# Kernel optimization log

Hardware: AMD Instinct MI355X
Metric: run time of the kernel (lower is better)

Reference implementation:

```python
import jax, jax.numpy as jnp
import numpy as np

N_NODES = 100000


def setup_inputs() -> dict:
    key = jax.random.key(0)
    k1, k2, k3, k4 = jax.random.split(key, 4)
    E = 1600000
    in_dim, out_dim = 256, 64
    h = jax.random.normal(k1, (N_NODES, in_dim), dtype=jnp.float32)
    src = jax.random.randint(k2, (E,), 0, N_NODES, dtype=jnp.int64)
    dst = jax.random.randint(k3, (E,), 0, N_NODES, dtype=jnp.int64)
    W = jax.random.normal(k4, (in_dim, out_dim), dtype=jnp.float32) * (1.0 / np.sqrt(in_dim))
    b = jnp.zeros((out_dim,), dtype=jnp.float32)
    return {"h": h, "src": src, "dst": dst, "W": W, "b": b}


def reference(h, src, dst, W, b):
    # dgl GraphConv, norm='both': out = D_in^{-1/2} A D_out^{-1/2} h W + b
    E = src.shape[0]
    ones = jnp.ones((E,), dtype=h.dtype)
    deg_out = jax.ops.segment_sum(ones, src, num_segments=N_NODES)  # out-degree of src nodes
    deg_in = jax.ops.segment_sum(ones, dst, num_segments=N_NODES)   # in-degree of dst nodes
    norm_src = jnp.clip(deg_out, 1.0, None) ** -0.5                  # [N]
    norm_dst = jnp.clip(deg_in, 1.0, None) ** -0.5                   # [N]
    # in_dim > out_dim: project first (as dgl does), then aggregate small features
    x = (h * norm_src[:, None]) @ W                                  # [N, out_dim]
    msgs = x[src]                                                    # [E, out_dim] gather
    agg = jax.ops.segment_sum(msgs, dst, num_segments=N_NODES)      # [N, out_dim] scatter-add
    out = agg * norm_dst[:, None] + b
    # ReLU; dropout is identity in eval mode
    return jax.nn.relu(out)
```

## Files before the change

### kernel.cpp

```cpp
#include <hip/hip_runtime.h>
#include <hip/hip_fp16.h>

#define N_NODES 100000
#define IN_DIM 256
#define OUT_DIM 64
#define NT 782
#define NSC 512
#define SMAX 3200
#define CAP_F 3072
#define GEMM_BLKS 1563

typedef _Float16 half8 __attribute__((ext_vector_type(8)));
typedef float f32x4 __attribute__((ext_vector_type(4)));

__global__ __launch_bounds__(256) void init_kernel(int* __restrict__ cursorD,
                                                   int* __restrict__ cursorS) {
    int i = blockIdx.x * 256 + threadIdx.x;
    if (i < NT) { cursorD[i] = 0; cursorS[i] = 0; }
}

#define A_LD 136
__global__ __launch_bounds__(256) void fused_kernel(const int* __restrict__ src,
                                                    const int* __restrict__ dst,
                                                    int* __restrict__ cursorD,
                                                    int* __restrict__ cursorS,
                                                    int* __restrict__ binnedD,
                                                    unsigned char* __restrict__ srcb,
                                                    const float* __restrict__ hmat,
                                                    const float* __restrict__ W,
                                                    __half* __restrict__ xh,
                                                    int E, int chunk) {
    __shared__ char smem[47568];
    const int t = threadIdx.x;
    if (blockIdx.x < NSC) {
        int* sorted            = (int*)(smem);
        int* histD             = (int*)(smem + 12800);
        int* boffD             = (int*)(smem + 15928);
        int* resvD             = (int*)(smem + 19056);
        int* histS             = (int*)(smem + 22184);
        int* boffS             = (int*)(smem + 25312);
        int* resvS             = (int*)(smem + 28440);
        unsigned short* sbin   = (unsigned short*)(smem + 31568);
        unsigned short* sbinS  = (unsigned short*)(smem + 37968);
        unsigned char* sortedB = (unsigned char*)(smem + 44368);
        const int blk = blockIdx.x;
        const int lane = t & 63, wv = t >> 6;
        const int lo = blk * chunk;
        int hiA = lo + chunk; if (hiA > E) hiA = E;
        for (int s0 = lo; s0 < hiA; s0 += SMAX) {
            int m = hiA - s0; if (m > SMAX) m = SMAX;
            for (int i = t; i < NT; i += 256) { histD[i] = 0; histS[i] = 0; }
            __syncthreads();
            for (int k = t; k < m; k += 256) {
                int s = src[s0 + k], d = dst[s0 + k];
                atomicAdd(&histD[d >> 7], 1);
                atomicAdd(&histS[s >> 7], 1);
            }
            __syncthreads();
            if (wv < 2) {
                int* hsrc = (wv == 0) ? histD : histS;
                int* bdst = (wv == 0) ? boffD : boffS;
                int carry = 0;
                for (int r = 0; r < (NT + 63) / 64; ++r) {
                    int i = r * 64 + lane;
                    int v = (i < NT) ? hsrc[i] : 0;
                    int incl = v;
#pragma unroll
                    for (int off = 1; off < 64; off <<= 1) {
                        int y = __shfl_up(incl, off);
                        if (lane >= off) incl += y;
                    }
                    if (i < NT) bdst[i] = carry + incl - v;
                    carry += __shfl(incl, 63);
                }
            }
            __syncthreads();
            for (int i = t; i < NT; i += 256) {
                int hd = histD[i];
                if (hd) resvD[i] = atomicAdd(&cursorD[i], hd);
                int hs = histS[i];
                if (hs) resvS[i] = atomicAdd(&cursorS[i], hs);
                histD[i] = boffD[i];
                histS[i] = boffS[i];
            }
            __syncthreads();
            for (int k = t; k < m; k += 256) {
                int s = src[s0 + k], d = dst[s0 + k];
                int bd = d >> 7;
                int p = atomicAdd(&histD[bd], 1);
                sorted[p] = (s << 7) | (d & 127);
                sbin[p] = (unsigned short)bd;
                int bs = s >> 7;
                int ps = atomicAdd(&histS[bs], 1);
                sortedB[ps] = (unsigned char)(s & 127);
                sbinS[ps] = (unsigned short)bs;
            }
            __syncthreads();
            for (int k = t; k < m; k += 256) {
                int b = sbin[k];
                int loc = resvD[b] + (k - boffD[b]);
                if (loc < CAP_F) binnedD[b * CAP_F + loc] = sorted[k];
                int bs = sbinS[k];
                int locS = resvS[bs] + (k - boffS[bs]);
                if (locS < CAP_F) srcb[bs * CAP_F + locS] = sortedB[k];
            }
            __syncthreads();
        }
    } else {
        _Float16* sA = (_Float16*)(smem);
        _Float16* sB = (_Float16*)(smem + 64 * A_LD * 2);
        const int lane = t & 63;
        const int w = t >> 6;
        const int row0 = (blockIdx.x - NSC) * 64;
        const int m0 = (w & 1) * 32;
        const int n0 = (w >> 1) * 32;

        f32x4 acc00 = {0.f, 0.f, 0.f, 0.f}, acc01 = {0.f, 0.f, 0.f, 0.f};
        f32x4 acc10 = {0.f, 0.f, 0.f, 0.f}, acc11 = {0.f, 0.f, 0.f, 0.f};

        for (int khalf = 0; khalf < 2; ++khalf) {
            const int k0 = khalf * 128;
            __syncthreads();
#pragma unroll
            for (int it = 0; it < 8; ++it) {
                int f = t + it * 256;
                int row = f >> 5;
                int c4 = f & 31;
                int grow = row0 + row; if (grow >= N_NODES) grow = N_NODES - 1;
                float4 v = *(const float4*)(hmat + (size_t)grow * IN_DIM + k0 + c4 * 4);
                _Float16 p[4];
                p[0] = (_Float16)v.x; p[1] = (_Float16)v.y;
                p[2] = (_Float16)v.z; p[3] = (_Float16)v.w;
                *(uint2*)&sA[row * A_LD + c4 * 4] = *(uint2*)p;
            }
            {
                int n = t & 63;
                int kk0 = (t >> 6) * 32;
#pragma unroll
                for (int kb = 0; kb < 8; ++kb) {
                    _Float16 p[4];
#pragma unroll
                    for (int u = 0; u < 4; ++u)
                        p[u] = (_Float16)W[(size_t)(k0 + kk0 + kb * 4 + u) * OUT_DIM + n];
                    *(uint2*)&sB[n * A_LD + kk0 + kb * 4] = *(uint2*)p;
                }
            }
            __syncthreads();
#pragma unroll
            for (int kb = 0; kb < 4; ++kb) {
                int koff = kb * 32 + (lane >> 4) * 8;
                half8 a0 = *(const half8*)&sA[(m0 + (lane & 15)) * A_LD + koff];
                half8 a1 = *(const half8*)&sA[(m0 + 16 + (lane & 15)) * A_LD + koff];
                half8 b0 = *(const half8*)&sB[(n0 + (lane & 15)) * A_LD + koff];
                half8 b1 = *(const half8*)&sB[(n0 + 16 + (lane & 15)) * A_LD + koff];
                acc00 = __builtin_amdgcn_mfma_f32_16x16x32_f16(a0, b0, acc00, 0, 0, 0);
                acc01 = __builtin_amdgcn_mfma_f32_16x16x32_f16(a0, b1, acc01, 0, 0, 0);
                acc10 = __builtin_amdgcn_mfma_f32_16x16x32_f16(a1, b0, acc10, 0, 0, 0);
                acc11 = __builtin_amdgcn_mfma_f32_16x16x32_f16(a1, b1, acc11, 0, 0, 0);
            }
        }

        const int col16 = lane & 15;
        const int rq = (lane >> 4) * 4;
#pragma unroll
        for (int mi = 0; mi < 2; ++mi) {
#pragma unroll
            for (int ni = 0; ni < 2; ++ni) {
                const f32x4 a = (mi == 0) ? (ni == 0 ? acc00 : acc01)
                                          : (ni == 0 ? acc10 : acc11);
                int col = n0 + ni * 16 + col16;
#pragma unroll
                for (int r = 0; r < 4; ++r) {
                    int row = row0 + m0 + mi * 16 + rq + r;
                    if (row < N_NODES)
                        xh[(size_t)row * OUT_DIM + col] = __float2half(a[r]);
                }
            }
        }
    }
}

__global__ __launch_bounds__(256) void tile_kernel(const int* __restrict__ cursorD,
                                                   const int* __restrict__ cursorS,
                                                   const int* __restrict__ binnedD,
                                                   const unsigned char* __restrict__ srcb,
                                                   int* __restrict__ csr,
                                                   int* __restrict__ offs, int* __restrict__ cnt,
                                                   float* __restrict__ nrmS) {
    __shared__ int h[128], cur[128];
    __shared__ int lcsr[CAP_F];
    __shared__ int w0tot;
    const int bin = blockIdx.x, t = threadIdx.x, lane = t & 63;
    if (t < 128) h[t] = 0;
    __syncthreads();

    const int base = bin * CAP_F;
    int m = cursorD[bin]; if (m > CAP_F) m = CAP_F;
    for (int k = t; k < m; k += 256) atomicAdd(&h[binnedD[base + k] & 127], 1);
    __syncthreads();
    int v = (t < 128) ? h[t] : 0;
    int incl = v;
#pragma unroll
    for (int off = 1; off < 64; off <<= 1) {
        int y = __shfl_up(incl, off);
        if (lane >= off) incl += y;
    }
    if (t == 63) w0tot = incl;
    __syncthreads();
    int excl = incl - v + ((t >= 64 && t < 128) ? w0tot : 0);
    if (t < 128) {
        cur[t] = excl;
        int node = bin * 128 + t;
        if (node < N_NODES) { offs[node] = base + excl; cnt[node] = v; }
    }
    __syncthreads();
    for (int k = t; k < m; k += 256) {
        int rec = binnedD[base + k];
        int p = atomicAdd(&cur[rec & 127], 1);
        lcsr[p] = rec >> 7;
    }
    __syncthreads();
    for (int k = t; k < m; k += 256) csr[base + k] = lcsr[k];

    __syncthreads();
    if (t < 128) h[t] = 0;
    __syncthreads();
    int ms = cursorS[bin]; if (ms > CAP_F) ms = CAP_F;
    const int sbase = bin * CAP_F;
    for (int k = t; k < ms; k += 256) atomicAdd(&h[srcb[sbase + k]], 1);
    __syncthreads();
    if (t < 128) {
        int node = bin * 128 + t;
        if (node < N_NODES) {
            int d = h[t];
            nrmS[node] = rsqrtf((float)(d < 1 ? 1 : d));
        }
    }
}

__global__ __launch_bounds__(256) void aggregate_kernel(const int* __restrict__ offs,
                                                        const int* __restrict__ cnt,
                                                        const int* __restrict__ csr,
                                                        const float* __restrict__ nrmS,
                                                        const __half* __restrict__ xh,
                                                        const float* __restrict__ b,
                                                        float* __restrict__ out) {
    const int t = threadIdx.x;
    const int lane = t & 63;
    const int wid = t >> 6;
    const int node = blockIdx.x * 4 + wid;
    const int g = lane >> 3;
    const int c = lane & 7;

    const int start = offs[node];
    const int n = cnt[node];

    float acc[8] = {0.f, 0.f, 0.f, 0.f, 0.f, 0.f, 0.f, 0.f};
    for (int base = 0; base < n; base += 64) {
        int k = base + lane;
        int sidx = (k < n) ? csr[start + k] : 0;
        int m = n - base; if (m > 64) m = 64;
        for (int e0 = 0; e0 < m; e0 += 16) {
            int ea = e0 + g;
            int eb = e0 + 8 + g;
            int sa = __shfl(sidx, ea);
            int sb = __shfl(sidx, eb);
            bool va = ea < m;
            bool vb = eb < m;
            float wa = va ? nrmS[sa] : 0.f;
            uint4 ra = *(const uint4*)(xh + (size_t)(va ? sa : 0) * OUT_DIM + 8 * c);
            const bool grpb = (e0 + 8) < m;
            uint4 rb;
            float wb = 0.f;
            if (grpb) {
                wb = vb ? nrmS[sb] : 0.f;
                rb = *(const uint4*)(xh + (size_t)(vb ? sb : 0) * OUT_DIM + 8 * c);
            }
            {
                const __half2* hp = (const __half2*)&ra;
#pragma unroll
                for (int p = 0; p < 4; ++p) {
                    float2 f = __half22float2(hp[p]);
                    acc[2 * p]     = fmaf(wa, f.x, acc[2 * p]);
                    acc[2 * p + 1] = fmaf(wa, f.y, acc[2 * p + 1]);
                }
            }
            if (grpb) {
                const __half2* hp = (const __half2*)&rb;
#pragma unroll
                for (int p = 0; p < 4; ++p) {
                    float2 f = __half22float2(hp[p]);
                    acc[2 * p]     = fmaf(wb, f.x, acc[2 * p]);
                    acc[2 * p + 1] = fmaf(wb, f.y, acc[2 * p + 1]);
                }
            }
        }
    }

#pragma unroll
    for (int off = 8; off < 64; off <<= 1) {
#pragma unroll
        for (int p = 0; p < 8; ++p)
            acc[p] += __shfl_xor(acc[p], off);
    }

    if (g == 0) {
        float nrm = rsqrtf((float)(n < 1 ? 1 : n));
        float4 bv0 = *(const float4*)&b[c * 8];
        float4 bv1 = *(const float4*)&b[c * 8 + 4];
        float4 r0, r1;
        r0.x = fmaxf(fmaf(acc[0], nrm, bv0.x), 0.f);
        r0.y = fmaxf(fmaf(acc[1], nrm, bv0.y), 0.f);
        r0.z = fmaxf(fmaf(acc[2], nrm, bv0.z), 0.f);
        r0.w = fmaxf(fmaf(acc[3], nrm, bv0.w), 0.f);
        r1.x = fmaxf(fmaf(acc[4], nrm, bv1.x), 0.f);
        r1.y = fmaxf(fmaf(acc[5], nrm, bv1.y), 0.f);
        r1.z = fmaxf(fmaf(acc[6], nrm, bv1.z), 0.f);
        r1.w = fmaxf(fmaf(acc[7], nrm, bv1.w), 0.f);
        float4* orow = (float4*)(out + (size_t)node * OUT_DIM + c * 8);
        orow[0] = r0;
        orow[1] = r1;
    }
}

extern "C" void kernel_launch(void* const* d_in, const int* in_sizes, int n_in,
                              void* d_out, int out_size, void* d_ws, size_t ws_size,
                              hipStream_t stream) {
    const float* h   = (const float*)d_in[0];
    const int*   src = (const int*)d_in[1];
    const int*   dst = (const int*)d_in[2];
    const float* W   = (const float*)d_in[3];
    const float* b   = (const float*)d_in[4];
    float* out = (float*)d_out;
    const int E = in_sizes[1];
    const int chunkS = (E + NSC - 1) / NSC;

    char* ws = (char*)d_ws;
    int*           cursorD = (int*)(ws);
    int*           cursorS = (int*)(ws + 3328);
    int*           binnedD = (int*)(ws + 6656);
    int*           csr     = binnedD;
    unsigned char* srcb    = (unsigned char*)(ws + 9615872);
    int*           offs    = (int*)(ws + 12018176);
    int*           cntA    = (int*)(ws + 12418176);
    float*         nrmS    = (float*)(ws + 12818176);
    __half*        xh      = (__half*)(ws + 13218176);

    init_kernel<<<4, 256, 0, stream>>>(cursorD, cursorS);
    fused_kernel<<<NSC + GEMM_BLKS, 256, 0, stream>>>(src, dst, cursorD, cursorS,
                                                      binnedD, srcb, h, W, xh, E, chunkS);
    tile_kernel<<<NT, 256, 0, stream>>>(cursorD, cursorS, binnedD, srcb, csr, offs, cntA, nrmS);
    aggregate_kernel<<<N_NODES / 4, 256, 0, stream>>>(offs, cntA, csr, nrmS, xh, b, out);
}
```

Measured before the change: 253.6 us.

## Move GEMM from scatter kernel into the per-bin CSR build kernel

The edge binning pass becomes a standalone scatter kernel, and the projection GEMM now shares a launch with the per-bin CSR and degree-normalisation pass instead of with the scatter. The aim is to give the GEMM blocks a lighter companion that uses less LDS, and to keep the scatter blocks from competing with GEMM blocks for occupancy. The number of launches stays the same. GEMM blocks now use 34.8 KB of LDS while the tile branch needs about 13 KB, so the fused kernel's occupancy is set by the larger of the two.

Measured after the change: 259.3 us. 1.02x slower.

```diff
diff --git a/kernel.cpp b/kernel.cpp
--- a/kernel.cpp
+++ b/kernel.cpp
@@ -9,6 +9,8 @@
 #define SMAX 3200
 #define CAP_F 3072
 #define GEMM_BLKS 1563
+#define A_LD 136
+#define FUSED2_LDS (64 * A_LD * 2 * 2)
 
 typedef _Float16 half8 __attribute__((ext_vector_type(8)));
 typedef float f32x4 __attribute__((ext_vector_type(4)));
@@ -19,99 +21,152 @@
     if (i < NT) { cursorD[i] = 0; cursorS[i] = 0; }
 }
 
-#define A_LD 136
-__global__ __launch_bounds__(256) void fused_kernel(const int* __restrict__ src,
-                                                    const int* __restrict__ dst,
-                                                    int* __restrict__ cursorD,
-                                                    int* __restrict__ cursorS,
-                                                    int* __restrict__ binnedD,
-                                                    unsigned char* __restrict__ srcb,
-                                                    const float* __restrict__ hmat,
-                                                    const float* __restrict__ W,
-                                                    __half* __restrict__ xh,
-                                                    int E, int chunk) {
-    __shared__ char smem[47568];
+__global__ __launch_bounds__(256) void scatter_kernel(const int* __restrict__ src,
+                                                      const int* __restrict__ dst,
+                                                      int* __restrict__ cursorD,
+                                                      int* __restrict__ cursorS,
+                                                      int* __restrict__ binnedD,
+                                                      unsigned char* __restrict__ srcb,
+                                                      int E, int chunk) {
+    __shared__ int sorted[SMAX];
+    __shared__ unsigned short sbin[SMAX];
+    __shared__ unsigned char sortedB[SMAX];
+    __shared__ unsigned short sbinS[SMAX];
+    __shared__ int histD[NT], boffD[NT], resvD[NT];
+    __shared__ int histS[NT], boffS[NT], resvS[NT];
+    const int t = threadIdx.x, blk = blockIdx.x;
+    const int lane = t & 63, wv = t >> 6;
+    const int lo = blk * chunk;
+    int hiA = lo + chunk; if (hiA > E) hiA = E;
+    for (int s0 = lo; s0 < hiA; s0 += SMAX) {
+        int m = hiA - s0; if (m > SMAX) m = SMAX;
+        for (int i = t; i < NT; i += 256) { histD[i] = 0; histS[i] = 0; }
+        __syncthreads();
+        for (int k = t; k < m; k += 256) {
+            int s = src[s0 + k], d = dst[s0 + k];
+            atomicAdd(&histD[d >> 7], 1);
+            atomicAdd(&histS[s >> 7], 1);
+        }
+        __syncthreads();
+        if (wv < 2) {
+            int* hsrc = (wv == 0) ? histD : histS;
+            int* bdst = (wv == 0) ? boffD : boffS;
+            int carry = 0;
+            for (int r = 0; r < (NT + 63) / 64; ++r) {
+                int i = r * 64 + lane;
+                int v = (i < NT) ? hsrc[i] : 0;
+                int incl = v;
+#pragma unroll
+                for (int off = 1; off < 64; off <<= 1) {
+                    int y = __shfl_up(incl, off);
+                    if (lane >= off) incl += y;
+                }
+                if (i < NT) bdst[i] = carry + incl - v;
+                carry += __shfl(incl, 63);
+            }
+        }
+        __syncthreads();
+        for (int i = t; i < NT; i += 256) {
+            int hd = histD[i];
+            if (hd) resvD[i] = atomicAdd(&cursorD[i], hd);
+            int hs = histS[i];
+            if (hs) resvS[i] = atomicAdd(&cursorS[i], hs);
+            histD[i] = boffD[i];
+            histS[i] = boffS[i];
+        }
+        __syncthreads();
+        for (int k = t; k < m; k += 256) {
+            int s = src[s0 + k], d = dst[s0 + k];
+            int bd = d >> 7;
+            int p = atomicAdd(&histD[bd], 1);
+            sorted[p] = (s << 7) | (d & 127);
+            sbin[p] = (unsigned short)bd;
+            int bs = s >> 7;
+            int ps = atomicAdd(&histS[bs], 1);
+            sortedB[ps] = (unsigned char)(s & 127);
+            sbinS[ps] = (unsigned short)bs;
+        }
+        __syncthreads();
+        for (int k = t; k < m; k += 256) {
+            int b = sbin[k];
+            int loc = resvD[b] + (k - boffD[b]);
+            if (loc < CAP_F) binnedD[b * CAP_F + loc] = sorted[k];
+            int bs = sbinS[k];
+            int locS = resvS[bs] + (k - boffS[bs]);
+            if (locS < CAP_F) srcb[bs * CAP_F + locS] = sortedB[k];
+        }
+        __syncthreads();
+    }
+}
+
+__global__ __launch_bounds__(256) void fused2_kernel(const int* __restrict__ cursorD,
+                                                     const int* __restrict__ cursorS,
+                                                     int* __restrict__ binnedD,
+                                                     const unsigned char* __restrict__ srcb,
+                                                     int* __restrict__ offs, int* __restrict__ cnt,
+                                                     float* __restrict__ nrmS,
+                                                     const float* __restrict__ hmat,
+                                                     const float* __restrict__ W,
+                                                     __half* __restrict__ xh) {
+    __shared__ char smem[FUSED2_LDS];
     const int t = threadIdx.x;
-    if (blockIdx.x < NSC) {
-        int* sorted            = (int*)(smem);
-        int* histD             = (int*)(smem + 12800);
-        int* boffD             = (int*)(smem + 15928);
-        int* resvD             = (int*)(smem + 19056);
-        int* histS             = (int*)(smem + 22184);
-        int* boffS             = (int*)(smem + 25312);
-        int* resvS             = (int*)(smem + 28440);
-        unsigned short* sbin   = (unsigned short*)(smem + 31568);
-        unsigned short* sbinS  = (unsigned short*)(smem + 37968);
-        unsigned char* sortedB = (unsigned char*)(smem + 44368);
-        const int blk = blockIdx.x;
-        const int lane = t & 63, wv = t >> 6;
-        const int lo = blk * chunk;
-        int hiA = lo + chunk; if (hiA > E) hiA = E;
-        for (int s0 = lo; s0 < hiA; s0 += SMAX) {
-            int m = hiA - s0; if (m > SMAX) m = SMAX;
-            for (int i = t; i < NT; i += 256) { histD[i] = 0; histS[i] = 0; }
-            __syncthreads();
-            for (int k = t; k < m; k += 256) {
-                int s = src[s0 + k], d = dst[s0 + k];
-                atomicAdd(&histD[d >> 7], 1);
-                atomicAdd(&histS[s >> 7], 1);
-            }
-            __syncthreads();
-            if (wv < 2) {
-                int* hsrc = (wv == 0) ? histD : histS;
-                int* bdst = (wv == 0) ? boffD : boffS;
-                int carry = 0;
-                for (int r = 0; r < (NT + 63) / 64; ++r) {
-                    int i = r * 64 + lane;
-                    int v = (i < NT) ? hsrc[i] : 0;
-                    int incl = v;
-#pragma unroll
-                    for (int off = 1; off < 64; off <<= 1) {
-                        int y = __shfl_up(incl, off);
-                        if (lane >= off) incl += y;
-                    }
-                    if (i < NT) bdst[i] = carry + incl - v;
-                    carry += __shfl(incl, 63);
-                }
-            }
-            __syncthreads();
-            for (int i = t; i < NT; i += 256) {
-                int hd = histD[i];
-                if (hd) resvD[i] = atomicAdd(&cursorD[i], hd);
-                int hs = histS[i];
-                if (hs) resvS[i] = atomicAdd(&cursorS[i], hs);
-                histD[i] = boffD[i];
-                histS[i] = boffS[i];
-            }
-            __syncthreads();
-            for (int k = t; k < m; k += 256) {
-                int s = src[s0 + k], d = dst[s0 + k];
-                int bd = d >> 7;
-                int p = atomicAdd(&histD[bd], 1);
-                sorted[p] = (s << 7) | (d & 127);
-                sbin[p] = (unsigned short)bd;
-                int bs = s >> 7;
-                int ps = atomicAdd(&histS[bs], 1);
-                sortedB[ps] = (unsigned char)(s & 127);
-                sbinS[ps] = (unsigned short)bs;
-            }
-            __syncthreads();
-            for (int k = t; k < m; k += 256) {
-                int b = sbin[k];
-                int loc = resvD[b] + (k - boffD[b]);
-                if (loc < CAP_F) binnedD[b * CAP_F + loc] = sorted[k];
-                int bs = sbinS[k];
-                int locS = resvS[bs] + (k - boffS[bs]);
-                if (locS < CAP_F) srcb[bs * CAP_F + locS] = sortedB[k];
-            }
-            __syncthreads();
+    if (blockIdx.x < NT) {
+        int* h    = (int*)(smem);
+        int* cur  = (int*)(smem + 512);
+        int* lcsr = (int*)(smem + 1024);
+        int* w0t  = (int*)(smem + 13312);
+        const int bin = blockIdx.x, lane = t & 63;
+        if (t < 128) h[t] = 0;
+        __syncthreads();
+
+        const int base = bin * CAP_F;
+        int m = cursorD[bin]; if (m > CAP_F) m = CAP_F;
+        for (int k = t; k < m; k += 256) atomicAdd(&h[binnedD[base + k] & 127], 1);
+        __syncthreads();
+        int v = (t < 128) ? h[t] : 0;
+        int incl = v;
+#pragma unroll
+        for (int off = 1; off < 64; off <<= 1) {
+            int y = __shfl_up(incl, off);
+            if (lane >= off) incl += y;
+        }
+        if (t == 63) *w0t = incl;
+        __syncthreads();
+        int excl = incl - v + ((t >= 64 && t < 128) ? *w0t : 0);
+        if (t < 128) {
+            cur[t] = excl;
+            int node = bin * 128 + t;
+            if (node < N_NODES) { offs[node] = base + excl; cnt[node] = v; }
+        }
+        __syncthreads();
+        for (int k = t; k < m; k += 256) {
+            int rec = binnedD[base + k];
+            int p = atomicAdd(&cur[rec & 127], 1);
+            lcsr[p] = rec >> 7;
+        }
+        __syncthreads();
+        for (int k = t; k < m; k += 256) binnedD[base + k] = lcsr[k];
+
+        __syncthreads();
+        if (t < 128) h[t] = 0;
+        __syncthreads();
+        int ms = cursorS[bin]; if (ms > CAP_F) ms = CAP_F;
+        const int sbase = bin * CAP_F;
+        for (int k = t; k < ms; k += 256) atomicAdd(&h[srcb[sbase + k]], 1);
+        __syncthreads();
+        if (t < 128) {
+            int node = bin * 128 + t;
+            if (node < N_NODES) {
+                int d = h[t];
+                nrmS[node] = rsqrtf((float)(d < 1 ? 1 : d));
+            }
         }
     } else {
         _Float16* sA = (_Float16*)(smem);
         _Float16* sB = (_Float16*)(smem + 64 * A_LD * 2);
         const int lane = t & 63;
         const int w = t >> 6;
-        const int row0 = (blockIdx.x - NSC) * 64;
+        const int row0 = (blockIdx.x - NT) * 64;
         const int m0 = (w & 1) * 32;
         const int n0 = (w >> 1) * 32;
 
@@ -176,64 +231,6 @@
                         xh[(size_t)row * OUT_DIM + col] = __float2half(a[r]);
                 }
             }
-        }
-    }
-}
-
-__global__ __launch_bounds__(256) void tile_kernel(const int* __restrict__ cursorD,
-                                                   const int* __restrict__ cursorS,
-                                                   const int* __restrict__ binnedD,
-                                                   const unsigned char* __restrict__ srcb,
-                                                   int* __restrict__ csr,
-                                                   int* __restrict__ offs, int* __restrict__ cnt,
-                                                   float* __restrict__ nrmS) {
-    __shared__ int h[128], cur[128];
-    __shared__ int lcsr[CAP_F];
-    __shared__ int w0tot;
-    const int bin = blockIdx.x, t = threadIdx.x, lane = t & 63;
-    if (t < 128) h[t] = 0;
-    __syncthreads();
-
-    const int base = bin * CAP_F;
-    int m = cursorD[bin]; if (m > CAP_F) m = CAP_F;
-    for (int k = t; k < m; k += 256) atomicAdd(&h[binnedD[base + k] & 127], 1);
-    __syncthreads();
-    int v = (t < 128) ? h[t] : 0;
-    int incl = v;
-#pragma unroll
-    for (int off = 1; off < 64; off <<= 1) {
-        int y = __shfl_up(incl, off);
-        if (lane >= off) incl += y;
-    }
-    if (t == 63) w0tot = incl;
-    __syncthreads();
-    int excl = incl - v + ((t >= 64 && t < 128) ? w0tot : 0);
-    if (t < 128) {
-        cur[t] = excl;
-        int node = bin * 128 + t;
-        if (node < N_NODES) { offs[node] = base + excl; cnt[node] = v; }
-    }
-    __syncthreads();
-    for (int k = t; k < m; k += 256) {
-        int rec = binnedD[base + k];
-        int p = atomicAdd(&cur[rec & 127], 1);
-        lcsr[p] = rec >> 7;
-    }
-    __syncthreads();
-    for (int k = t; k < m; k += 256) csr[base + k] = lcsr[k];
-
-    __syncthreads();
-    if (t < 128) h[t] = 0;
-    __syncthreads();
-    int ms = cursorS[bin]; if (ms > CAP_F) ms = CAP_F;
-    const int sbase = bin * CAP_F;
-    for (int k = t; k < ms; k += 256) atomicAdd(&h[srcb[sbase + k]], 1);
-    __syncthreads();
-    if (t < 128) {
-        int node = bin * 128 + t;
-        if (node < N_NODES) {
-            int d = h[t];
-            nrmS[node] = rsqrtf((float)(d < 1 ? 1 : d));
         }
     }
 }
@@ -347,8 +344,8 @@
     __half*        xh      = (__half*)(ws + 13218176);
 
     init_kernel<<<4, 256, 0, stream>>>(cursorD, cursorS);
-    fused_kernel<<<NSC + GEMM_BLKS, 256, 0, stream>>>(src, dst, cursorD, cursorS,
-                                                      binnedD, srcb, h, W, xh, E, chunkS);
-    tile_kernel<<<NT, 256, 0, stream>>>(cursorD, cursorS, binnedD, srcb, csr, offs, cntA, nrmS);
+    scatter_kernel<<<NSC, 256, 0, stream>>>(src, dst, cursorD, cursorS, binnedD, srcb, E, chunkS);
+    fused2_kernel<<<NT + GEMM_BLKS, 256, 0, stream>>>(cursorD, cursorS, binnedD, srcb,
+                                                      offs, cntA, nrmS, h, W, xh);
     aggregate_kernel<<<N_NODES / 4, 256, 0, stream>>>(offs, cntA, csr, nrmS, xh, b, out);
 }
```
